# Kernel optimization log

Hardware: AMD Instinct MI355X
Metric: run time of the kernel (lower is better)

The kernel has to match this reference:

```python
import jax, jax.numpy as jnp
import numpy as np

N = 131072
H = 768

def setup_inputs() -> dict:
    key = jax.random.key(0)
    k1, k2, k3, k4 = jax.random.split(key, 4)
    h_i = jax.random.normal(k1, (N, H), dtype=jnp.float32)
    W_weight = jax.random.normal(k2, (H, H), dtype=jnp.float32) * 0.02
    W_bias = jax.random.normal(k3, (H,), dtype=jnp.float32) * 0.02
    v = jax.random.normal(k4, (1, H), dtype=jnp.float32) * 0.1
    return {"h_i": h_i, "W_weight": W_weight, "W_bias": W_bias, "v": v}

def reference(h_i, W_weight, W_bias, v):
    # u_i = tanh(Linear(h_i)) : [N, H]
    u_i = jnp.tanh(h_i @ W_weight.T + W_bias)
    # scores = v @ u_i.T : [1, N]
    scores = v @ u_i.T
    alpha = jax.nn.softmax(scores, axis=1)  # [1, N]
    # weighted sum over N -> [1, H]
    return alpha @ h_i
```

## Files before the change

kernel.cpp:

```cpp
#include <hip/hip_runtime.h>

#define HDIM 768
#define BM 64
#define NCHUNK 24
#define CHALF 24576
#define A_STRIDE 1536
#define ASWZ(row) (((row) & 7) << 4)

typedef _Float16 f16x8 __attribute__((ext_vector_type(8)));
typedef _Float16 f16x4 __attribute__((ext_vector_type(4)));
typedef float f32x4 __attribute__((ext_vector_type(4)));

#define LDS_A     0
#define LDS_BIAS  98304
#define LDS_V     101376
#define LDS_SRED  104448
#define LDS_E     108544
#define LDS_TOTAL 108800

#define WS_WT    0
#define WS_Z     1179648
#define WS_PART  1179712
#define WS_PART2 7471168
#define WS_NEED  (WS_PART2 + 49152)

__device__ __forceinline__ float tanh_fast(float z) {
    float e2 = __expf(2.0f * z);
    return 1.0f - 2.0f / (e2 + 1.0f);
}

__device__ __forceinline__ f16x8 cvt8(f32x4 x0, f32x4 x1) {
    f16x8 f;
    f[0] = (_Float16)x0[0]; f[1] = (_Float16)x0[1];
    f[2] = (_Float16)x0[2]; f[3] = (_Float16)x0[3];
    f[4] = (_Float16)x1[0]; f[5] = (_Float16)x1[1];
    f[6] = (_Float16)x1[2]; f[7] = (_Float16)x1[3];
    return f;
}

__global__ __launch_bounds__(1024) void prep_kernel(
    const float* __restrict__ W, _Float16* __restrict__ Wt,
    float* __restrict__ Z, float* __restrict__ accbuf) {
    int idx = blockIdx.x * 1024 + threadIdx.x;
    if (idx < 73728) {
        int c  = idx / 96;
        int r  = idx - c * 96;
        int kc = r >> 2;
        int q  = r & 3;
        const float* src = W + c * HDIM + kc * 32 + q * 8;
        f16x8 v = cvt8(*(const f32x4*)src, *(const f32x4*)(src + 4));
        *(f16x8*)(Wt + (size_t)kc * CHALF + c * 32 + q * 8) = v;
    }
    if (idx < HDIM) accbuf[idx] = 0.0f;
    if (idx == 0) *Z = 0.0f;
}

__global__ __launch_bounds__(1024, 4) void score_fused_kernel(
    const float* __restrict__ h, const _Float16* __restrict__ Wt,
    const float* __restrict__ bias, const float* __restrict__ vvec,
    float* __restrict__ part, float* __restrict__ accbuf,
    float* __restrict__ Z, int use_part) {

    extern __shared__ char smem[];
    float* bias_s = (float*)(smem + LDS_BIAS);
    float* v_s    = (float*)(smem + LDS_V);
    float* s_red  = (float*)(smem + LDS_SRED);
    float* e_lds  = (float*)(smem + LDS_E);

    const int tid  = threadIdx.x;
    const int wave = tid >> 6;
    const int lane = tid & 63;
    const int l15  = lane & 15;
    const int lhi  = lane >> 4;
    const int row0 = blockIdx.x * BM;

    if (tid < HDIM) { bias_s[tid] = bias[tid]; v_s[tid] = vvec[tid]; }

    const _Float16* wtp = Wt + (wave * 48 + l15) * 32 + lhi * 8;
    const int aswz = ASWZ(l15);

    if (tid < 512) {
        int r = tid >> 3, k4 = tid & 7;
        f32x4 x = __builtin_nontemporal_load(
            (const f32x4*)(h + (size_t)(row0 + r) * HDIM + k4 * 4));
        f16x4 v;
        v[0] = (_Float16)x[0]; v[1] = (_Float16)x[1];
        v[2] = (_Float16)x[2]; v[3] = (_Float16)x[3];
        *(f16x4*)(smem + LDS_A + r * A_STRIDE + ((k4 * 8) ^ ASWZ(r))) = v;
    }
    f32x4 paA = {0.f, 0.f, 0.f, 0.f}, paB = {0.f, 0.f, 0.f, 0.f};
    if (tid < 512)
        paA = __builtin_nontemporal_load(
            (const f32x4*)(h + (size_t)(row0 + (tid >> 3)) * HDIM + 32 + (tid & 7) * 4));
    f16x8 bA0 = *(const f16x8*)(wtp);
    f16x8 bA1 = *(const f16x8*)(wtp + 512);
    f16x8 bA2 = *(const f16x8*)(wtp + 1024);
    f16x8 bB0, bB1, bB2;
    __syncthreads();

    f32x4 acc[4][3];
    #pragma unroll
    for (int rt = 0; rt < 4; ++rt)
        #pragma unroll
        for (int ct = 0; ct < 3; ++ct)
            acc[rt][ct] = (f32x4){0.f, 0.f, 0.f, 0.f};

#define CHUNK(KC, BC0, BC1, BC2, BN0, BN1, BN2, PAW, PAL)                              \
    {                                                                                   \
        const char* ab = smem + LDS_A + l15 * A_STRIDE + (((KC) * 64 + lhi * 16) ^ aswz); \
        f16x8 a0 = *(const f16x8*)(ab);                                                 \
        f16x8 a1 = *(const f16x8*)(ab + 16 * A_STRIDE);                                 \
        f16x8 a2 = *(const f16x8*)(ab + 32 * A_STRIDE);                                 \
        f16x8 a3 = *(const f16x8*)(ab + 48 * A_STRIDE);                                 \
        if ((KC) + 1 < NCHUNK) {                                                        \
            const _Float16* wp = wtp + (size_t)((KC) + 1) * CHALF;                      \
            BN0 = *(const f16x8*)(wp);                                                  \
            BN1 = *(const f16x8*)(wp + 512);                                            \
            BN2 = *(const f16x8*)(wp + 1024);                                           \
        }                                                                               \
        if ((KC) + 2 < NCHUNK && tid < 512)                                             \
            PAL = __builtin_nontemporal_load(                                           \
                (const f32x4*)(h + (size_t)(row0 + (tid >> 3)) * HDIM                   \
                               + ((KC) + 2) * 32 + (tid & 7) * 4));                     \
        acc[0][0] = __builtin_amdgcn_mfma_f32_16x16x32_f16(a0, BC0, acc[0][0], 0, 0, 0); \
        acc[0][1] = __builtin_amdgcn_mfma_f32_16x16x32_f16(a0, BC1, acc[0][1], 0, 0, 0); \
        acc[0][2] = __builtin_amdgcn_mfma_f32_16x16x32_f16(a0, BC2, acc[0][2], 0, 0, 0); \
        acc[1][0] = __builtin_amdgcn_mfma_f32_16x16x32_f16(a1, BC0, acc[1][0], 0, 0, 0); \
        acc[1][1] = __builtin_amdgcn_mfma_f32_16x16x32_f16(a1, BC1, acc[1][1], 0, 0, 0); \
        acc[1][2] = __builtin_amdgcn_mfma_f32_16x16x32_f16(a1, BC2, acc[1][2], 0, 0, 0); \
        acc[2][0] = __builtin_amdgcn_mfma_f32_16x16x32_f16(a2, BC0, acc[2][0], 0, 0, 0); \
        acc[2][1] = __builtin_amdgcn_mfma_f32_16x16x32_f16(a2, BC1, acc[2][1], 0, 0, 0); \
        acc[2][2] = __builtin_amdgcn_mfma_f32_16x16x32_f16(a2, BC2, acc[2][2], 0, 0, 0); \
        acc[3][0] = __builtin_amdgcn_mfma_f32_16x16x32_f16(a3, BC0, acc[3][0], 0, 0, 0); \
        acc[3][1] = __builtin_amdgcn_mfma_f32_16x16x32_f16(a3, BC1, acc[3][1], 0, 0, 0); \
        acc[3][2] = __builtin_amdgcn_mfma_f32_16x16x32_f16(a3, BC2, acc[3][2], 0, 0, 0); \
        if ((KC) + 1 < NCHUNK && tid < 512) {                                           \
            int r_ = tid >> 3;                                                          \
            f16x4 v_;                                                                   \
            v_[0] = (_Float16)PAW[0]; v_[1] = (_Float16)PAW[1];                         \
            v_[2] = (_Float16)PAW[2]; v_[3] = (_Float16)PAW[3];                         \
            *(f16x4*)(smem + LDS_A + r_ * A_STRIDE                                      \
                      + ((((KC) + 1) * 64 + (tid & 7) * 8) ^ ASWZ(r_))) = v_;           \
        }                                                                               \
        asm volatile("s_waitcnt lgkmcnt(0)" ::: "memory");                              \
        __builtin_amdgcn_s_barrier();                                                   \
    }

    for (int k2 = 0; k2 < NCHUNK; k2 += 2) {
        CHUNK(k2,     bA0, bA1, bA2, bB0, bB1, bB2, paA, paB)
        CHUNK(k2 + 1, bB0, bB1, bB2, bA0, bA1, bA2, paB, paA)
    }
#undef CHUNK

    __syncthreads();

    float pr[4][4];
    #pragma unroll
    for (int rt = 0; rt < 4; ++rt)
        #pragma unroll
        for (int r = 0; r < 4; ++r) pr[rt][r] = 0.f;

    #pragma unroll
    for (int ct = 0; ct < 3; ++ct) {
        int col = wave * 48 + ct * 16 + l15;
        float bj = bias_s[col];
        float vj = v_s[col];
        #pragma unroll
        for (int rt = 0; rt < 4; ++rt)
            #pragma unroll
            for (int r = 0; r < 4; ++r)
                pr[rt][r] = fmaf(vj, tanh_fast(acc[rt][ct][r] + bj), pr[rt][r]);
    }
    #pragma unroll
    for (int rt = 0; rt < 4; ++rt)
        #pragma unroll
        for (int r = 0; r < 4; ++r) {
            float x = pr[rt][r];
            x += __shfl_xor(x, 1);
            x += __shfl_xor(x, 2);
            x += __shfl_xor(x, 4);
            x += __shfl_xor(x, 8);
            if (l15 == 0) s_red[wave * 64 + rt * 16 + lhi * 4 + r] = x;
        }
    __syncthreads();

    if (tid < 64) {
        float s = 0.f;
        #pragma unroll
        for (int w = 0; w < 16; ++w) s += s_red[w * 64 + tid];
        float e = __expf(s);
        e_lds[tid] = e;
        float tot = e;
        tot += __shfl_xor(tot, 1);
        tot += __shfl_xor(tot, 2);
        tot += __shfl_xor(tot, 4);
        tot += __shfl_xor(tot, 8);
        tot += __shfl_xor(tot, 16);
        tot += __shfl_xor(tot, 32);
        if (tid == 0) atomicAdd(Z, tot);
    }
    __syncthreads();

    if (tid < HDIM) {
        float s = 0.f;
        #pragma unroll 8
        for (int i = 0; i < BM; ++i) {
            const _Float16* ap = (const _Float16*)(smem + LDS_A + i * A_STRIDE
                                                   + ((tid * 2) ^ ASWZ(i)));
            s += e_lds[i] * (float)(*ap);
        }
        if (use_part) part[(size_t)blockIdx.x * HDIM + tid] = s;
        else          atomicAdd(accbuf + tid, s);
    }
}

__global__ __launch_bounds__(128) void fin1_kernel(
    const float* __restrict__ part, float* __restrict__ part2) {
    const int g  = blockIdx.x / 6;
    const int cb = blockIdx.x % 6;
    const int col = cb * 128 + threadIdx.x;
    float s = 0.f;
    #pragma unroll 8
    for (int p = g * 128; p < (g + 1) * 128; ++p) s += part[(size_t)p * HDIM + col];
    part2[g * HDIM + col] = s;
}

__global__ __launch_bounds__(128) void fin2_kernel(
    const float* __restrict__ src, const float* __restrict__ Z,
    float* __restrict__ out, int ngroups) {
    const int col = blockIdx.x * 128 + threadIdx.x;
    float s = 0.f;
    for (int g = 0; g < ngroups; ++g) s += src[g * HDIM + col];
    out[col] = s / (*Z);
}

extern "C" void kernel_launch(void* const* d_in, const int* in_sizes, int n_in,
                              void* d_out, int out_size, void* d_ws, size_t ws_size,
                              hipStream_t stream) {
    const float* h    = (const float*)d_in[0];
    const float* W    = (const float*)d_in[1];
    const float* bias = (const float*)d_in[2];
    const float* vv   = (const float*)d_in[3];
    float* out = (float*)d_out;

    const int n = in_sizes[0] / HDIM;

    char* ws = (char*)d_ws;
    _Float16* Wt  = (_Float16*)(ws + WS_WT);
    float* Z      = (float*)(ws + WS_Z);
    float* part   = (float*)(ws + WS_PART);
    float* part2  = (float*)(ws + WS_PART2);
    float* accbuf = (float*)(ws + WS_PART);

    const int use_part = (ws_size >= (size_t)WS_NEED) ? 1 : 0;

    hipFuncSetAttribute((const void*)score_fused_kernel,
                        hipFuncAttributeMaxDynamicSharedMemorySize, LDS_TOTAL);

    prep_kernel<<<72, 1024, 0, stream>>>(W, Wt, Z, accbuf);

    score_fused_kernel<<<n / BM, 1024, LDS_TOTAL, stream>>>(
        h, Wt, bias, vv, part, accbuf, Z, use_part);

    if (use_part) {
        fin1_kernel<<<96, 128, 0, stream>>>(part, part2);
        fin2_kernel<<<HDIM / 128, 128, 0, stream>>>(part2, Z, out, 16);
    } else {
        fin2_kernel<<<HDIM / 128, 128, 0, stream>>>(accbuf, Z, out, 1);
    }
}
```

Before: 288.6 us.

## Load full A tile upfront, drop per-chunk barriers, pad LDS stride instead of swizzle

The 64x768 h tile is now converted to fp16 and staged into LDS in one bulk prologue using all threads, replacing the streamed per-chunk A loads. This removes the per-chunk LDS writes, s_waitcnt and s_barrier from the MFMA loop. The XOR swizzle is replaced by a padded row stride, and the final weighted-sum stage reads f16x2 pairs with half the threads. In exchange, global h loads no longer overlap with MFMA work, and LDS usage grows slightly, which could reduce occupancy or expose load latency.

```diff
diff --git a/kernel.cpp b/kernel.cpp
--- a/kernel.cpp
+++ b/kernel.cpp
@@ -4,19 +4,19 @@
 #define BM 64
 #define NCHUNK 24
 #define CHALF 24576
-#define A_STRIDE 1536
-#define ASWZ(row) (((row) & 7) << 4)
+#define A_STRIDE 1552
 
 typedef _Float16 f16x8 __attribute__((ext_vector_type(8)));
 typedef _Float16 f16x4 __attribute__((ext_vector_type(4)));
+typedef _Float16 f16x2 __attribute__((ext_vector_type(2)));
 typedef float f32x4 __attribute__((ext_vector_type(4)));
 
 #define LDS_A     0
-#define LDS_BIAS  98304
-#define LDS_V     101376
-#define LDS_SRED  104448
-#define LDS_E     108544
-#define LDS_TOTAL 108800
+#define LDS_BIAS  99328
+#define LDS_V     102400
+#define LDS_SRED  105472
+#define LDS_E     109568
+#define LDS_TOTAL 109824
 
 #define WS_WT    0
 #define WS_Z     1179648
@@ -76,26 +76,25 @@
 
     if (tid < HDIM) { bias_s[tid] = bias[tid]; v_s[tid] = vvec[tid]; }
 
-    const _Float16* wtp = Wt + (wave * 48 + l15) * 32 + lhi * 8;
-    const int aswz = ASWZ(l15);
-
-    if (tid < 512) {
-        int r = tid >> 3, k4 = tid & 7;
+    #pragma unroll
+    for (int i = 0; i < 12; ++i) {
+        int flat = i * 1024 + tid;
+        int r  = flat / 192;
+        int c4 = flat - r * 192;
         f32x4 x = __builtin_nontemporal_load(
-            (const f32x4*)(h + (size_t)(row0 + r) * HDIM + k4 * 4));
+            (const f32x4*)(h + (size_t)(row0 + r) * HDIM + c4 * 4));
         f16x4 v;
         v[0] = (_Float16)x[0]; v[1] = (_Float16)x[1];
         v[2] = (_Float16)x[2]; v[3] = (_Float16)x[3];
-        *(f16x4*)(smem + LDS_A + r * A_STRIDE + ((k4 * 8) ^ ASWZ(r))) = v;
-    }
-    f32x4 paA = {0.f, 0.f, 0.f, 0.f}, paB = {0.f, 0.f, 0.f, 0.f};
-    if (tid < 512)
-        paA = __builtin_nontemporal_load(
-            (const f32x4*)(h + (size_t)(row0 + (tid >> 3)) * HDIM + 32 + (tid & 7) * 4));
-    f16x8 bA0 = *(const f16x8*)(wtp);
-    f16x8 bA1 = *(const f16x8*)(wtp + 512);
-    f16x8 bA2 = *(const f16x8*)(wtp + 1024);
+        *(f16x4*)(smem + LDS_A + r * A_STRIDE + c4 * 8) = v;
+    }
+
+    const _Float16* wcur = Wt + (wave * 48 + l15) * 32 + lhi * 8;
+    f16x8 bA0 = *(const f16x8*)(wcur);
+    f16x8 bA1 = *(const f16x8*)(wcur + 512);
+    f16x8 bA2 = *(const f16x8*)(wcur + 1024);
     f16x8 bB0, bB1, bB2;
+
     __syncthreads();
 
     f32x4 acc[4][3];
@@ -105,23 +104,19 @@
         for (int ct = 0; ct < 3; ++ct)
             acc[rt][ct] = (f32x4){0.f, 0.f, 0.f, 0.f};
 
-#define CHUNK(KC, BC0, BC1, BC2, BN0, BN1, BN2, PAW, PAL)                              \
-    {                                                                                   \
-        const char* ab = smem + LDS_A + l15 * A_STRIDE + (((KC) * 64 + lhi * 16) ^ aswz); \
-        f16x8 a0 = *(const f16x8*)(ab);                                                 \
-        f16x8 a1 = *(const f16x8*)(ab + 16 * A_STRIDE);                                 \
-        f16x8 a2 = *(const f16x8*)(ab + 32 * A_STRIDE);                                 \
-        f16x8 a3 = *(const f16x8*)(ab + 48 * A_STRIDE);                                 \
-        if ((KC) + 1 < NCHUNK) {                                                        \
-            const _Float16* wp = wtp + (size_t)((KC) + 1) * CHALF;                      \
-            BN0 = *(const f16x8*)(wp);                                                  \
-            BN1 = *(const f16x8*)(wp + 512);                                            \
-            BN2 = *(const f16x8*)(wp + 1024);                                           \
-        }                                                                               \
-        if ((KC) + 2 < NCHUNK && tid < 512)                                             \
-            PAL = __builtin_nontemporal_load(                                           \
-                (const f32x4*)(h + (size_t)(row0 + (tid >> 3)) * HDIM                   \
-                               + ((KC) + 2) * 32 + (tid & 7) * 4));                     \
+    const char* aBase = smem + LDS_A + l15 * A_STRIDE + lhi * 16;
+
+#define CHUNK(KOFF, PF, BC0, BC1, BC2, BN0, BN1, BN2)                                    \
+    {                                                                                    \
+        const _Float16* wn = wcur + (PF) * CHALF;                                        \
+        BN0 = *(const f16x8*)(wn);                                                       \
+        BN1 = *(const f16x8*)(wn + 512);                                                 \
+        BN2 = *(const f16x8*)(wn + 1024);                                                \
+        const char* ab = aBase + (KOFF);                                                 \
+        f16x8 a0 = *(const f16x8*)(ab);                                                  \
+        f16x8 a1 = *(const f16x8*)(ab + 16 * A_STRIDE);                                  \
+        f16x8 a2 = *(const f16x8*)(ab + 32 * A_STRIDE);                                  \
+        f16x8 a3 = *(const f16x8*)(ab + 48 * A_STRIDE);                                  \
         acc[0][0] = __builtin_amdgcn_mfma_f32_16x16x32_f16(a0, BC0, acc[0][0], 0, 0, 0); \
         acc[0][1] = __builtin_amdgcn_mfma_f32_16x16x32_f16(a0, BC1, acc[0][1], 0, 0, 0); \
         acc[0][2] = __builtin_amdgcn_mfma_f32_16x16x32_f16(a0, BC2, acc[0][2], 0, 0, 0); \
@@ -134,25 +129,15 @@
         acc[3][0] = __builtin_amdgcn_mfma_f32_16x16x32_f16(a3, BC0, acc[3][0], 0, 0, 0); \
         acc[3][1] = __builtin_amdgcn_mfma_f32_16x16x32_f16(a3, BC1, acc[3][1], 0, 0, 0); \
         acc[3][2] = __builtin_amdgcn_mfma_f32_16x16x32_f16(a3, BC2, acc[3][2], 0, 0, 0); \
-        if ((KC) + 1 < NCHUNK && tid < 512) {                                           \
-            int r_ = tid >> 3;                                                          \
-            f16x4 v_;                                                                   \
-            v_[0] = (_Float16)PAW[0]; v_[1] = (_Float16)PAW[1];                         \
-            v_[2] = (_Float16)PAW[2]; v_[3] = (_Float16)PAW[3];                         \
-            *(f16x4*)(smem + LDS_A + r_ * A_STRIDE                                      \
-                      + ((((KC) + 1) * 64 + (tid & 7) * 8) ^ ASWZ(r_))) = v_;           \
-        }                                                                               \
-        asm volatile("s_waitcnt lgkmcnt(0)" ::: "memory");                              \
-        __builtin_amdgcn_s_barrier();                                                   \
-    }
-
+    }
+
+    #pragma unroll 1
     for (int k2 = 0; k2 < NCHUNK; k2 += 2) {
-        CHUNK(k2,     bA0, bA1, bA2, bB0, bB1, bB2, paA, paB)
-        CHUNK(k2 + 1, bB0, bB1, bB2, bA0, bA1, bA2, paB, paA)
+        CHUNK(k2 * 64,      1, bA0, bA1, bA2, bB0, bB1, bB2)
+        CHUNK(k2 * 64 + 64, 2, bB0, bB1, bB2, bA0, bA1, bA2)
+        wcur += 2 * CHALF;
     }
 #undef CHUNK
-
-    __syncthreads();
 
     float pr[4][4];
     #pragma unroll
@@ -201,16 +186,22 @@
     }
     __syncthreads();
 
-    if (tid < HDIM) {
-        float s = 0.f;
+    if (tid < 384) {
+        float s0 = 0.f, s1 = 0.f;
         #pragma unroll 8
         for (int i = 0; i < BM; ++i) {
-            const _Float16* ap = (const _Float16*)(smem + LDS_A + i * A_STRIDE
-                                                   + ((tid * 2) ^ ASWZ(i)));
-            s += e_lds[i] * (float)(*ap);
+            f16x2 a2 = *(const f16x2*)(smem + LDS_A + i * A_STRIDE + tid * 4);
+            float e = e_lds[i];
+            s0 = fmaf(e, (float)a2[0], s0);
+            s1 = fmaf(e, (float)a2[1], s1);
         }
-        if (use_part) part[(size_t)blockIdx.x * HDIM + tid] = s;
-        else          atomicAdd(accbuf + tid, s);
+        if (use_part) {
+            float* dst = part + (size_t)blockIdx.x * HDIM + tid * 2;
+            dst[0] = s0; dst[1] = s1;
+        } else {
+            atomicAdd(accbuf + tid * 2, s0);
+            atomicAdd(accbuf + tid * 2 + 1, s1);
+        }
     }
 }
 
```

Measured after the change: 288.8 us. Within noise of the previous version (+0.1%).
